# Performance work log

Measured on AMD Instinct MI355X. Metric: run time of the kernel, lower is better.

The kernel has to match this reference:

```python
import jax, jax.numpy as jnp
import numpy as np

DIM = 1024
NUM_HEADS = 16
HEAD_DIM = DIM // NUM_HEADS
TGT_LEN = 4096


def setup_inputs() -> dict:
    key = jax.random.key(0)
    k1, k2, k3 = jax.random.split(key, 3)
    x = jax.random.normal(k1, (TGT_LEN, DIM), dtype=jnp.float32)
    W_in = jax.random.normal(k2, (3 * DIM, DIM), dtype=jnp.float32) * (DIM ** -0.5)
    W_out = jax.random.normal(k3, (DIM, DIM), dtype=jnp.float32) * (DIM ** -0.5)
    return {"x": x, "W_in": W_in, "W_out": W_out, "tgt_len": TGT_LEN}


def reference(x, W_in, W_out, tgt_len):
    # QKV projection (torch Linear: y = x @ W^T)
    qkv = x @ W_in.T  # [T, 3*dim]
    q, k, v = jnp.split(qkv, 3, axis=-1)
    # [T, dim] -> [H, T, hd]
    q = q.reshape(tgt_len, NUM_HEADS, HEAD_DIM).transpose(1, 0, 2)
    k = k.reshape(tgt_len, NUM_HEADS, HEAD_DIM).transpose(1, 0, 2)
    v = v.reshape(tgt_len, NUM_HEADS, HEAD_DIM).transpose(1, 0, 2)
    scaling = HEAD_DIM ** -0.5
    scores = jnp.einsum('htd,hsd->hts', q, k) * scaling  # [H, T, T]
    # joint softmax over the full (T, T) matrix per head (NOT row-wise)
    maxes = jnp.max(scores, axis=(1, 2), keepdims=True)
    x_exp = jnp.exp(scores - maxes)
    probs = x_exp / jnp.sum(x_exp, axis=(1, 2), keepdims=True)
    attn = jnp.einsum('hts,hsd->htd', probs, v)  # [H, T, hd]
    attn = attn.transpose(1, 0, 2).reshape(tgt_len, DIM)
    return attn @ W_out.T
```

## Files before the change

### kernel.cpp

```cpp
#include <hip/hip_runtime.h>

#define TLEN 4096
#define DIM 1024
#define NHEAD 16
#define HDIM 64
#define QKV_COLS (3 * DIM)
#define QSCALE 0.1803368801111244f
#define NCHUNK 2
#define SCHUNK (TLEN / NCHUNK)

typedef __attribute__((ext_vector_type(8))) short short8;
typedef __attribute__((ext_vector_type(4))) float f32x4;

struct alignas(8) s4 { short v[4]; };

__device__ float g_Lsum[NHEAD];
__device__ float g_recipL[NHEAD];

__global__ void zeroL() {
    if (threadIdx.x < NHEAD) g_Lsum[threadIdx.x] = 0.0f;
}
__global__ void recipL() {
    if (threadIdx.x < NHEAD) g_recipL[threadIdx.x] = 1.0f / g_Lsum[threadIdx.x];
}

__device__ __forceinline__ unsigned bf16_rtne_bits(float x) {
    unsigned u = __float_as_uint(x);
    return (u + 0x7fffu + ((u >> 16) & 1u)) >> 16;
}

__device__ __forceinline__ void cp16(const short* g, short* l) {
    __builtin_amdgcn_global_load_lds(
        (const __attribute__((address_space(1))) unsigned int*)g,
        (__attribute__((address_space(3))) unsigned int*)l,
        16, 0, 0);
}

__global__ __launch_bounds__(256) void conv_bf16(
    const float* __restrict__ src, short* __restrict__ dst, int n4)
{
    int i = blockIdx.x * 256 + threadIdx.x;
    if (i < n4) {
        float4 v = ((const float4*)src)[i];
        s4 o;
        o.v[0] = (short)bf16_rtne_bits(v.x);
        o.v[1] = (short)bf16_rtne_bits(v.y);
        o.v[2] = (short)bf16_rtne_bits(v.z);
        o.v[3] = (short)bf16_rtne_bits(v.w);
        ((s4*)dst)[i] = o;
    }
}

__global__ __launch_bounds__(256) void conv_wout(
    const float* __restrict__ src, short* __restrict__ dst)
{
    int i = blockIdx.x * 256 + threadIdx.x;
    float s = g_recipL[(i & 255) >> 4];
    float4 v = ((const float4*)src)[i];
    s4 o;
    o.v[0] = (short)bf16_rtne_bits(v.x * s);
    o.v[1] = (short)bf16_rtne_bits(v.y * s);
    o.v[2] = (short)bf16_rtne_bits(v.z * s);
    o.v[3] = (short)bf16_rtne_bits(v.w * s);
    ((s4*)dst)[i] = o;
}

__global__ __launch_bounds__(256) void combine(
    const short* __restrict__ p0, const short* __restrict__ p1,
    short* __restrict__ dst, int n4)
{
    int i = blockIdx.x * 256 + threadIdx.x;
    if (i < n4) {
        s4 a = ((const s4*)p0)[i];
        s4 b = ((const s4*)p1)[i];
        s4 o;
#pragma unroll
        for (int m = 0; m < 4; ++m) {
            float fa = __uint_as_float(((unsigned)(unsigned short)a.v[m]) << 16);
            float fb = __uint_as_float(((unsigned)(unsigned short)b.v[m]) << 16);
            o.v[m] = (short)bf16_rtne_bits(fa + fb);
        }
        ((s4*)dst)[i] = o;
    }
}

template <bool OUT_BF16, bool SCALE_Q>
__global__ __launch_bounds__(256) void gemm_bt(
    const short* __restrict__ A, const short* __restrict__ B,
    void* __restrict__ Cout, int M, int N, int K)
{
    __shared__ __align__(16) short As[128][32];
    __shared__ __align__(16) short Bs[128][32];
    const int tid  = threadIdx.x;
    const int wv   = tid >> 6, lane = tid & 63;
    const int fr   = lane & 15, quad = lane >> 4;
    const int wm   = (wv >> 1) * 64, wn = (wv & 1) * 64;
    const int m0 = blockIdx.x * 128, n0 = blockIdx.y * 128;

    f32x4 acc[4][4] = {};

    for (int k0 = 0; k0 < K; k0 += 32) {
        __syncthreads();
#pragma unroll
        for (int c = tid; c < 512; c += 256) {
            int row = c >> 2, col = (c & 3) * 8;
            cp16(A + (size_t)(m0 + row) * K + k0 + col, &As[row][col]);
            cp16(B + (size_t)(n0 + row) * K + k0 + col, &Bs[row][col]);
        }
        __syncthreads();

        short8 af[4], bfr[4];
#pragma unroll
        for (int i = 0; i < 4; ++i) {
            af[i]  = *(const short8*)&As[wm + i * 16 + fr][quad * 8];
            bfr[i] = *(const short8*)&Bs[wn + i * 16 + fr][quad * 8];
        }
#pragma unroll
        for (int i = 0; i < 4; ++i)
#pragma unroll
            for (int j = 0; j < 4; ++j)
                acc[i][j] = __builtin_amdgcn_mfma_f32_16x16x32_bf16(af[i], bfr[j], acc[i][j], 0, 0, 0);
    }

    const float sc = (SCALE_Q && n0 < DIM) ? QSCALE : 1.0f;
#pragma unroll
    for (int i = 0; i < 4; ++i)
#pragma unroll
        for (int j = 0; j < 4; ++j)
#pragma unroll
            for (int r = 0; r < 4; ++r) {
                size_t off = (size_t)(m0 + wm + i * 16 + quad * 4 + r) * N + n0 + wn + j * 16 + fr;
                float v = acc[i][j][r] * sc;
                if (OUT_BF16)
                    ((short*)Cout)[off] = (short)bf16_rtne_bits(v);
                else
                    ((float*)Cout)[off] = v;
            }
}

__global__ __launch_bounds__(256) void attn_mfma(
    const short* __restrict__ qkvb, short* __restrict__ part)
{
    __shared__ short Ks[64][72];
    __shared__ short Vt[64][72];
    __shared__ short Ps[128][72];
    __shared__ float red[256];

    const int tid = threadIdx.x;
    const int t0 = blockIdx.x * 128;
    const int h  = blockIdx.y;
    const int chunk = blockIdx.z;
    const int lr  = tid >> 2;
    const int lc4 = (tid & 3) << 2;
    const int wv   = tid >> 6;
    const int lane = tid & 63;
    const int fr   = lane & 15;
    const int quad = lane >> 4;
    const int tb   = wv * 32;

#pragma unroll
    for (int half = 0; half < 128; half += 64)
#pragma unroll
        for (int c0 = 0; c0 < HDIM; c0 += 16) {
            int d = c0 + lc4;
            *(s4*)&Ps[half + lr][d] =
                *(const s4*)(qkvb + (size_t)(t0 + half + lr) * QKV_COLS + h * HDIM + d);
        }
    __syncthreads();

    short8 qf[2][2];
#pragma unroll
    for (int jt = 0; jt < 2; ++jt)
#pragma unroll
        for (int kh = 0; kh < 2; ++kh)
            qf[jt][kh] = *(const short8*)&Ps[tb + jt * 16 + fr][kh * 32 + quad * 8];

    short8 ones;
#pragma unroll
    for (int m = 0; m < 8; ++m) ones[m] = (short)0x3F80;

    f32x4 oaccT[4][2] = {};
    f32x4 racc[2] = {};

    for (int s0 = chunk * SCHUNK; s0 < (chunk + 1) * SCHUNK; s0 += 64) {
        __syncthreads();
#pragma unroll
        for (int c0 = 0; c0 < HDIM; c0 += 16) {
            int d = c0 + lc4;
            *(s4*)&Ks[lr][d] =
                *(const s4*)(qkvb + (size_t)(s0 + lr) * QKV_COLS + DIM + h * HDIM + d);
            s4 vv = *(const s4*)(qkvb + (size_t)(s0 + lr) * QKV_COLS + 2 * DIM + h * HDIM + d);
            Vt[d + 0][lr] = vv.v[0];
            Vt[d + 1][lr] = vv.v[1];
            Vt[d + 2][lr] = vv.v[2];
            Vt[d + 3][lr] = vv.v[3];
        }
        __syncthreads();

#pragma unroll
        for (int i = 0; i < 4; ++i) {
            short8 ka0 = *(const short8*)&Ks[i * 16 + fr][quad * 8];
            short8 ka1 = *(const short8*)&Ks[i * 16 + fr][32 + quad * 8];
#pragma unroll
            for (int jt = 0; jt < 2; ++jt) {
                f32x4 acc = {};
                acc = __builtin_amdgcn_mfma_f32_16x16x32_bf16(ka0, qf[jt][0], acc, 0, 0, 0);
                acc = __builtin_amdgcn_mfma_f32_16x16x32_bf16(ka1, qf[jt][1], acc, 0, 0, 0);
                unsigned u0 = __float_as_uint(__builtin_amdgcn_exp2f(acc[0]));
                unsigned u1 = __float_as_uint(__builtin_amdgcn_exp2f(acc[1]));
                unsigned u2 = __float_as_uint(__builtin_amdgcn_exp2f(acc[2]));
                unsigned u3 = __float_as_uint(__builtin_amdgcn_exp2f(acc[3]));
                uint2 pk;
                pk.x = __builtin_amdgcn_perm(u1, u0, 0x07060302);
                pk.y = __builtin_amdgcn_perm(u3, u2, 0x07060302);
                *(uint2*)&Ps[tb + jt * 16 + fr][i * 16 + quad * 4] = pk;
            }
        }

        short8 pb[2][2];
#pragma unroll
        for (int jt = 0; jt < 2; ++jt)
#pragma unroll
            for (int kh = 0; kh < 2; ++kh)
                pb[jt][kh] = *(const short8*)&Ps[tb + jt * 16 + fr][kh * 32 + quad * 8];

#pragma unroll
        for (int jt = 0; jt < 2; ++jt) {
            racc[jt] = __builtin_amdgcn_mfma_f32_16x16x32_bf16(ones, pb[jt][0], racc[jt], 0, 0, 0);
            racc[jt] = __builtin_amdgcn_mfma_f32_16x16x32_bf16(ones, pb[jt][1], racc[jt], 0, 0, 0);
        }
#pragma unroll
        for (int jd = 0; jd < 4; ++jd) {
            short8 va0 = *(const short8*)&Vt[jd * 16 + fr][quad * 8];
            short8 va1 = *(const short8*)&Vt[jd * 16 + fr][32 + quad * 8];
#pragma unroll
            for (int jt = 0; jt < 2; ++jt) {
                oaccT[jd][jt] = __builtin_amdgcn_mfma_f32_16x16x32_bf16(va0, pb[jt][0], oaccT[jd][jt], 0, 0, 0);
                oaccT[jd][jt] = __builtin_amdgcn_mfma_f32_16x16x32_bf16(va1, pb[jt][1], oaccT[jd][jt], 0, 0, 0);
            }
        }
    }

    short* pc = part + (size_t)chunk * TLEN * DIM;
#pragma unroll
    for (int jt = 0; jt < 2; ++jt)
#pragma unroll
        for (int jd = 0; jd < 4; ++jd) {
            unsigned u0 = bf16_rtne_bits(oaccT[jd][jt][0]);
            unsigned u1 = bf16_rtne_bits(oaccT[jd][jt][1]);
            unsigned u2 = bf16_rtne_bits(oaccT[jd][jt][2]);
            unsigned u3 = bf16_rtne_bits(oaccT[jd][jt][3]);
            uint2 pk;
            pk.x = u0 | (u1 << 16);
            pk.y = u2 | (u3 << 16);
            *(uint2*)(pc + (size_t)(t0 + tb + jt * 16 + fr) * DIM + h * HDIM + jd * 16 + quad * 4) = pk;
        }

    red[tid] = (racc[0][0] + racc[1][0]) * 0.25f;
    __syncthreads();
    for (int off = 128; off > 0; off >>= 1) {
        if (tid < off) red[tid] += red[tid + off];
        __syncthreads();
    }
    if (tid == 0) atomicAdd(&g_Lsum[h], red[0]);
}

extern "C" void kernel_launch(void* const* d_in, const int* in_sizes, int n_in,
                              void* d_out, int out_size, void* d_ws, size_t ws_size,
                              hipStream_t stream)
{
    const float* x     = (const float*)d_in[0];
    const float* W_in  = (const float*)d_in[1];
    const float* W_out = (const float*)d_in[2];
    float* out = (float*)d_out;

    char* ws = (char*)d_ws;
    short* xb    = (short*)(ws);
    short* wib   = (short*)(ws + (8u << 20));
    short* wob   = (short*)(ws + (14u << 20));
    short* qkvb  = (short*)(ws + (16u << 20));
    short* part  = (short*)(ws + (40u << 20));
    short* attnb = xb;

    zeroL<<<1, 64, 0, stream>>>();

    conv_bf16<<<(TLEN * DIM / 4 + 255) / 256, 256, 0, stream>>>(x, xb, TLEN * DIM / 4);
    conv_bf16<<<(QKV_COLS * DIM / 4 + 255) / 256, 256, 0, stream>>>(W_in, wib, QKV_COLS * DIM / 4);

    gemm_bt<true, true><<<dim3(TLEN / 128, QKV_COLS / 128), 256, 0, stream>>>(
        xb, wib, qkvb, TLEN, QKV_COLS, DIM);

    attn_mfma<<<dim3(TLEN / 128, NHEAD, NCHUNK), 256, 0, stream>>>(qkvb, part);

    recipL<<<1, 64, 0, stream>>>();
    conv_wout<<<(DIM * DIM / 4 + 255) / 256, 256, 0, stream>>>(W_out, wob);

    combine<<<(TLEN * DIM / 4 + 255) / 256, 256, 0, stream>>>(
        part, part + (size_t)TLEN * DIM, attnb, TLEN * DIM / 4);

    gemm_bt<false, false><<<dim3(TLEN / 128, DIM / 128), 256, 0, stream>>>(
        attnb, wob, out, TLEN, DIM, DIM);
}
```

Baseline: 266.2 us.

## Write V transposed from QKV GEMM epilogue and vectorize attention tile loads

The QKV GEMM epilogue now writes the V third of its output transposed into a separate [DIM, TLEN] buffer using packed 4-element stores. The attention kernel can then load V tiles with wide 16-byte row copies instead of scalar transposing writes into shared memory. K and Q tile loads are widened to two 16-byte loads per thread. This removes the scalar LDS transpose in the inner loop. In exchange, the GEMM epilogue writes V with a strided pattern across rows, and the part buffer moves to a new workspace offset.

```diff
diff --git a/kernel.cpp b/kernel.cpp
--- a/kernel.cpp
+++ b/kernel.cpp
@@ -84,10 +84,10 @@
     }
 }
 
-template <bool OUT_BF16, bool SCALE_Q>
+template <bool QKV_MODE>
 __global__ __launch_bounds__(256) void gemm_bt(
     const short* __restrict__ A, const short* __restrict__ B,
-    void* __restrict__ Cout, int M, int N, int K)
+    void* __restrict__ Cout, short* __restrict__ Vout, int M, int N, int K)
 {
     __shared__ __align__(16) short As[128][32];
     __shared__ __align__(16) short Bs[128][32];
@@ -122,24 +122,49 @@
                 acc[i][j] = __builtin_amdgcn_mfma_f32_16x16x32_bf16(af[i], bfr[j], acc[i][j], 0, 0, 0);
     }
 
-    const float sc = (SCALE_Q && n0 < DIM) ? QSCALE : 1.0f;
-#pragma unroll
-    for (int i = 0; i < 4; ++i)
-#pragma unroll
-        for (int j = 0; j < 4; ++j)
-#pragma unroll
-            for (int r = 0; r < 4; ++r) {
-                size_t off = (size_t)(m0 + wm + i * 16 + quad * 4 + r) * N + n0 + wn + j * 16 + fr;
-                float v = acc[i][j][r] * sc;
-                if (OUT_BF16)
-                    ((short*)Cout)[off] = (short)bf16_rtne_bits(v);
-                else
-                    ((float*)Cout)[off] = v;
+    if (QKV_MODE && n0 >= 2 * DIM) {
+#pragma unroll
+        for (int i = 0; i < 4; ++i)
+#pragma unroll
+            for (int j = 0; j < 4; ++j) {
+                int n = n0 - 2 * DIM + wn + j * 16 + fr;
+                int m = m0 + wm + i * 16 + quad * 4;
+                unsigned u0 = bf16_rtne_bits(acc[i][j][0]);
+                unsigned u1 = bf16_rtne_bits(acc[i][j][1]);
+                unsigned u2 = bf16_rtne_bits(acc[i][j][2]);
+                unsigned u3 = bf16_rtne_bits(acc[i][j][3]);
+                uint2 pk;
+                pk.x = u0 | (u1 << 16);
+                pk.y = u2 | (u3 << 16);
+                *(uint2*)(Vout + (size_t)n * TLEN + m) = pk;
             }
+    } else if (QKV_MODE) {
+        const float sc = (n0 < DIM) ? QSCALE : 1.0f;
+#pragma unroll
+        for (int i = 0; i < 4; ++i)
+#pragma unroll
+            for (int j = 0; j < 4; ++j)
+#pragma unroll
+                for (int r = 0; r < 4; ++r) {
+                    size_t off = (size_t)(m0 + wm + i * 16 + quad * 4 + r) * N + n0 + wn + j * 16 + fr;
+                    ((short*)Cout)[off] = (short)bf16_rtne_bits(acc[i][j][r] * sc);
+                }
+    } else {
+#pragma unroll
+        for (int i = 0; i < 4; ++i)
+#pragma unroll
+            for (int j = 0; j < 4; ++j)
+#pragma unroll
+                for (int r = 0; r < 4; ++r) {
+                    size_t off = (size_t)(m0 + wm + i * 16 + quad * 4 + r) * N + n0 + wn + j * 16 + fr;
+                    ((float*)Cout)[off] = acc[i][j][r];
+                }
+    }
 }
 
 __global__ __launch_bounds__(256) void attn_mfma(
-    const short* __restrict__ qkvb, short* __restrict__ part)
+    const short* __restrict__ qkvb, const short* __restrict__ vtb,
+    short* __restrict__ part)
 {
     __shared__ short Ks[64][72];
     __shared__ short Vt[64][72];
@@ -150,8 +175,8 @@
     const int t0 = blockIdx.x * 128;
     const int h  = blockIdx.y;
     const int chunk = blockIdx.z;
-    const int lr  = tid >> 2;
-    const int lc4 = (tid & 3) << 2;
+    const int srow = tid >> 2;
+    const int sch  = (tid & 3) * 16;
     const int wv   = tid >> 6;
     const int lane = tid & 63;
     const int fr   = lane & 15;
@@ -159,13 +184,13 @@
     const int tb   = wv * 32;
 
 #pragma unroll
-    for (int half = 0; half < 128; half += 64)
-#pragma unroll
-        for (int c0 = 0; c0 < HDIM; c0 += 16) {
-            int d = c0 + lc4;
-            *(s4*)&Ps[half + lr][d] =
-                *(const s4*)(qkvb + (size_t)(t0 + half + lr) * QKV_COLS + h * HDIM + d);
-        }
+    for (int half = 0; half < 128; half += 64) {
+        const short* src = qkvb + (size_t)(t0 + half + srow) * QKV_COLS + h * HDIM + sch;
+        uint4 a = *(const uint4*)(src);
+        uint4 b = *(const uint4*)(src + 8);
+        *(uint4*)&Ps[half + srow][sch]     = a;
+        *(uint4*)&Ps[half + srow][sch + 8] = b;
+    }
     __syncthreads();
 
     short8 qf[2][2];
@@ -184,16 +209,17 @@
 
     for (int s0 = chunk * SCHUNK; s0 < (chunk + 1) * SCHUNK; s0 += 64) {
         __syncthreads();
-#pragma unroll
-        for (int c0 = 0; c0 < HDIM; c0 += 16) {
-            int d = c0 + lc4;
-            *(s4*)&Ks[lr][d] =
-                *(const s4*)(qkvb + (size_t)(s0 + lr) * QKV_COLS + DIM + h * HDIM + d);
-            s4 vv = *(const s4*)(qkvb + (size_t)(s0 + lr) * QKV_COLS + 2 * DIM + h * HDIM + d);
-            Vt[d + 0][lr] = vv.v[0];
-            Vt[d + 1][lr] = vv.v[1];
-            Vt[d + 2][lr] = vv.v[2];
-            Vt[d + 3][lr] = vv.v[3];
+        {
+            const short* ksrc = qkvb + (size_t)(s0 + srow) * QKV_COLS + DIM + h * HDIM + sch;
+            uint4 ka = *(const uint4*)(ksrc);
+            uint4 kb = *(const uint4*)(ksrc + 8);
+            const short* vsrc = vtb + (size_t)(h * HDIM + srow) * TLEN + s0 + sch;
+            uint4 va = *(const uint4*)(vsrc);
+            uint4 vb = *(const uint4*)(vsrc + 8);
+            *(uint4*)&Ks[srow][sch]     = ka;
+            *(uint4*)&Ks[srow][sch + 8] = kb;
+            *(uint4*)&Vt[srow][sch]     = va;
+            *(uint4*)&Vt[srow][sch + 8] = vb;
         }
         __syncthreads();
 
@@ -279,7 +305,8 @@
     short* wib   = (short*)(ws + (8u << 20));
     short* wob   = (short*)(ws + (14u << 20));
     short* qkvb  = (short*)(ws + (16u << 20));
-    short* part  = (short*)(ws + (40u << 20));
+    short* vtb   = (short*)(ws + (40u << 20));
+    short* part  = (short*)(ws + (48u << 20));
     short* attnb = xb;
 
     zeroL<<<1, 64, 0, stream>>>();
@@ -287,10 +314,10 @@
     conv_bf16<<<(TLEN * DIM / 4 + 255) / 256, 256, 0, stream>>>(x, xb, TLEN * DIM / 4);
     conv_bf16<<<(QKV_COLS * DIM / 4 + 255) / 256, 256, 0, stream>>>(W_in, wib, QKV_COLS * DIM / 4);
 
-    gemm_bt<true, true><<<dim3(TLEN / 128, QKV_COLS / 128), 256, 0, stream>>>(
-        xb, wib, qkvb, TLEN, QKV_COLS, DIM);
-
-    attn_mfma<<<dim3(TLEN / 128, NHEAD, NCHUNK), 256, 0, stream>>>(qkvb, part);
+    gemm_bt<true><<<dim3(TLEN / 128, QKV_COLS / 128), 256, 0, stream>>>(
+        xb, wib, qkvb, vtb, TLEN, QKV_COLS, DIM);
+
+    attn_mfma<<<dim3(TLEN / 128, NHEAD, NCHUNK), 256, 0, stream>>>(qkvb, vtb, part);
 
     recipL<<<1, 64, 0, stream>>>();
     conv_wout<<<(DIM * DIM / 4 + 255) / 256, 256, 0, stream>>>(W_out, wob);
@@ -298,6 +325,6 @@
     combine<<<(TLEN * DIM / 4 + 255) / 256, 256, 0, stream>>>(
         part, part + (size_t)TLEN * DIM, attnb, TLEN * DIM / 4);
 
-    gemm_bt<false, false><<<dim3(TLEN / 128, DIM / 128), 256, 0, stream>>>(
-        attnb, wob, out, TLEN, DIM, DIM);
-}
+    gemm_bt<false><<<dim3(TLEN / 128, DIM / 128), 256, 0, stream>>>(
+        attnb, wob, out, nullptr, TLEN, DIM, DIM);
+}
```

Result: faster. 254.0 us (-4.6%).
